# Kernel tuning notes

Hardware: AMD Instinct MI355X
Metric: run time of the kernel (lower is better)

## Reference

```python
import math
import jax, jax.numpy as jnp
import numpy as np

N_NODES = 50000
N_EDGES = 600000
D = 128          # in_dim == out_dim
T = 4            # num_types
R = 4            # num_relations
H = 8            # n_heads
DK = D // H
MAX_LEN = 240    # RelTemporalEncoding max_len
EPS = 1e-5


def _sinusoid_table(n_hid, max_len):
    pos = jnp.arange(max_len, dtype=jnp.float32)[:, None]
    div = jnp.exp(jnp.arange(0, n_hid, 2, dtype=jnp.float32) * (-math.log(10000.0) / n_hid))
    s = jnp.sin(pos * div) / math.sqrt(n_hid)
    c = jnp.cos(pos * div) / math.sqrt(n_hid)
    emb = jnp.zeros((max_len, n_hid), dtype=jnp.float32)
    emb = emb.at[:, 0::2].set(s).at[:, 1::2].set(c)
    return emb


def setup_inputs() -> dict:
    key = jax.random.key(0)
    ks = jax.random.split(key, 24)
    f32 = jnp.float32
    inp = {
        'node_inp': jax.random.normal(ks[0], (N_NODES, D), dtype=f32),
        'node_type': jax.random.randint(ks[1], (N_NODES,), 0, T),
        'edge_index': jax.random.randint(ks[2], (2, N_EDGES), 0, N_NODES),
        'edge_type': jax.random.randint(ks[3], (N_EDGES,), 0, R),
        'edge_time': jax.random.randint(ks[4], (N_EDGES,), 0, MAX_LEN),
        # per-type Linear weights stored as [T, in, out] (x @ W + b)
        'Wk': jax.random.normal(ks[5], (T, D, D), dtype=f32) * 0.05,
        'bk': jnp.zeros((T, D), dtype=f32),
        'Wq': jax.random.normal(ks[6], (T, D, D), dtype=f32) * 0.05,
        'bq': jnp.zeros((T, D), dtype=f32),
        'Wv': jax.random.normal(ks[7], (T, D, D), dtype=f32) * 0.05,
        'bv': jnp.zeros((T, D), dtype=f32),
        'Wa': jax.random.normal(ks[8], (T, D, D), dtype=f32) * 0.05,
        'ba': jnp.zeros((T, D), dtype=f32),
        'gamma': jnp.ones((T, D), dtype=f32),
        'beta': jnp.zeros((T, D), dtype=f32),
        'rel_pri': jnp.ones((R, H), dtype=f32),
        'rel_att': jax.random.normal(ks[9], (R, H, DK, DK), dtype=f32) * 0.1,
        'rel_msg': jax.random.normal(ks[10], (R, H, DK, DK), dtype=f32) * 0.1,
        'skip': jnp.ones((T,), dtype=f32),
        'rte_W': jax.random.normal(ks[11], (D, D), dtype=f32) * 0.05,
        'rte_b': jnp.zeros((D,), dtype=f32),
    }
    return inp


def _type_proj(x, W, b, types):
    # all-type projection [T, N, D] then gather per-node type (T is small)
    allp = jnp.einsum('ni,tio->tno', x, W) + b[:, None, :]
    return allp[types, jnp.arange(x.shape[0])]


def reference(node_inp, node_type, edge_index, edge_type, edge_time,
              Wk, bk, Wq, bq, Wv, bv, Wa, ba, gamma, beta,
              rel_pri, rel_att, rel_msg, skip, rte_W, rte_b):
    N = node_inp.shape[0]
    E = edge_index.shape[1]
    src, tgt = edge_index[0], edge_index[1]  # j (source) -> i (target)

    # --- RelTemporalEncoding: x + Linear(emb[t]); emb is a fixed sinusoid table
    rte_out = _sinusoid_table(D, MAX_LEN) @ rte_W + rte_b  # [240, D]

    # --- per-node type-specific K/Q/V (linearity: K_t(x + rte) = K_t(x) + rte @ Wk_t)
    k_node = _type_proj(node_inp, Wk, bk, node_type)  # [N, D]
    v_node = _type_proj(node_inp, Wv, bv, node_type)
    q_node = _type_proj(node_inp, Wq, bq, node_type)
    k_rte = jnp.einsum('mi,tio->tmo', rte_out, Wk)  # [T, 240, D] (no bias; already in k_node)
    v_rte = jnp.einsum('mi,tio->tmo', rte_out, Wv)

    stype = node_type[src]
    k_e = (k_node[src] + k_rte[stype, edge_time]).reshape(E, H, DK)
    v_e = (v_node[src] + v_rte[stype, edge_time]).reshape(E, H, DK)
    q_e = q_node[tgt].reshape(E, H, DK)

    # --- per-relation head-wise transforms (R is small, fixed loop)
    k2 = jnp.zeros_like(k_e)
    msg = jnp.zeros_like(v_e)
    for r in range(R):
        sel = (edge_type == r)[:, None, None]
        k2 = jnp.where(sel, jnp.einsum('ehk,hkd->ehd', k_e, rel_att[r]), k2)
        msg = jnp.where(sel, jnp.einsum('ehk,hkd->ehd', v_e, rel_msg[r]), msg)

    logits = (q_e * k2).sum(-1) * rel_pri[edge_type] / math.sqrt(DK)  # [E, H]

    # --- softmax over edges grouped by target node
    m = jax.ops.segment_max(logits, tgt, num_segments=N)
    ex = jnp.exp(logits - m[tgt])
    den = jax.ops.segment_sum(ex, tgt, num_segments=N)
    att = ex / den[tgt]  # [E, H]

    res = (msg * att[..., None]).reshape(E, D)
    aggr = jax.ops.segment_sum(res, tgt, num_segments=N)  # [N, D]

    # --- update: per-type FFN + gated skip + per-type LayerNorm
    a = jax.nn.gelu(aggr, approximate=False)
    trans = _type_proj(a, Wa, ba, node_type)  # dropout p used in eval mode -> identity
    alpha = jax.nn.sigmoid(skip)[node_type][:, None]
    h = trans * alpha + node_inp * (1.0 - alpha)
    mu = h.mean(-1, keepdims=True)
    var = ((h - mu) ** 2).mean(-1, keepdims=True)
    out = (h - mu) / jnp.sqrt(var + EPS) * gamma[node_type] + beta[node_type]
    return out
```

## Files before the change

### kernel.cpp

```cpp
#include <hip/hip_runtime.h>
#include <hip/hip_fp16.h>
#include <math.h>

#define NH 8
#define NT 4
#define NR 4
#define MAXLEN 240

typedef __attribute__((ext_vector_type(8))) short bf16x8;
typedef __attribute__((ext_vector_type(4))) float f32x4;
typedef __attribute__((ext_vector_type(2))) float f32x2;

#if defined(__has_builtin)
#if __has_builtin(__builtin_amdgcn_cvt_pk_f32_fp8) && __has_builtin(__builtin_amdgcn_cvt_pk_fp8_f32)
#define HAS_HW_FP8 1
#endif
#endif

__device__ __forceinline__ unsigned short f2bf(float x) {
    unsigned u = __float_as_uint(x);
    u += 0x7fffu + ((u >> 16) & 1u);
    return (unsigned short)(u >> 16);
}
__device__ __forceinline__ float bflo(unsigned u) { return __uint_as_float(u << 16); }
__device__ __forceinline__ float bfhi(unsigned u) { return __uint_as_float(u & 0xffff0000u); }
__device__ __forceinline__ unsigned pack2(float a, float b) {
    return (unsigned)f2bf(a) | ((unsigned)f2bf(b) << 16);
}

__device__ __forceinline__ void fp8x4_dec(unsigned w, float* f) {
#ifdef HAS_HW_FP8
    f32x2 lo = __builtin_amdgcn_cvt_pk_f32_fp8(w, false);
    f32x2 hi = __builtin_amdgcn_cvt_pk_f32_fp8(w, true);
    f[0] = lo[0]; f[1] = lo[1]; f[2] = hi[0]; f[3] = hi[1];
#else
    unsigned ev = w & 0x00ff00ffu;
    unsigned od = (w >> 8) & 0x00ff00ffu;
    unsigned he = (((ev << 8) & 0x80008000u) | ((ev << 7) & 0x3f803f80u)) + 0x04000400u;
    unsigned ho = (((od << 8) & 0x80008000u) | ((od << 7) & 0x3f803f80u)) + 0x04000400u;
    __half2 h2e = *reinterpret_cast<__half2*>(&he);
    __half2 h2o = *reinterpret_cast<__half2*>(&ho);
    float2 fe = __half22float2(h2e);
    float2 fo = __half22float2(h2o);
    f[0] = fe.x; f[1] = fo.x; f[2] = fe.y; f[3] = fo.y;
#endif
}
__device__ __forceinline__ unsigned fp8x2_enc(float a, float b) {
#ifdef HAS_HW_FP8
    return (unsigned)__builtin_amdgcn_cvt_pk_fp8_f32(a, b, 0, false) & 0xffffu;
#else
    auto enc1 = [](float x) -> unsigned {
        float cl = fminf(fmaxf(x, -448.f), 448.f);
        __half h = __float2half(cl * 0.00390625f);
        unsigned short hr = *reinterpret_cast<unsigned short*>(&h);
        unsigned short rnd = (unsigned short)((hr & 0x7fff) + 0x3f + ((hr >> 7) & 1));
        return (unsigned)(((rnd >> 7) & 0x7f) | ((hr >> 8) & 0x80));
    };
    return enc1(a) | (enc1(b) << 8);
#endif
}

__global__ void zero_kernel(int* deg, int* cursor, int* dcnt, int* dcur, int N) {
    int i = blockIdx.x * blockDim.x + threadIdx.x;
    int stride = gridDim.x * blockDim.x;
    if (i < 256) { dcnt[i] = 0; dcur[i] = 0; }
    for (int j = i; j < N; j += stride) { deg[j] = 0; cursor[j] = 0; }
}

__global__ void deg_kernel(const int* __restrict__ ei, int* __restrict__ deg, int E) {
    int i = blockIdx.x * blockDim.x + threadIdx.x;
    int stride = gridDim.x * blockDim.x;
    for (int e = i; e < E; e += stride) atomicAdd(&deg[ei[E + e]], 1);
}

__global__ __launch_bounds__(256) void histA(const int* __restrict__ ntype,
                                             const int* __restrict__ deg,
                                             int* __restrict__ dcnt, int N) {
    __shared__ int h[256];
    int tid = threadIdx.x;
    h[tid] = 0;
    __syncthreads();
    int i = blockIdx.x * 256 + tid;
    if (i < N) atomicAdd(&h[ntype[i] * 64 + 63 - min(deg[i], 63)], 1);
    __syncthreads();
    if (h[tid]) atomicAdd(&dcnt[tid], h[tid]);
}

__global__ __launch_bounds__(256) void histB(const int* __restrict__ dcnt,
                                             int* __restrict__ dbase) {
    __shared__ int tmp[256];
    int v = dcnt[threadIdx.x];
    tmp[threadIdx.x] = v;
    __syncthreads();
    #pragma unroll
    for (int off = 1; off < 256; off <<= 1) {
        int t = threadIdx.x >= off ? tmp[threadIdx.x - off] : 0;
        __syncthreads();
        tmp[threadIdx.x] += t;
        __syncthreads();
    }
    dbase[threadIdx.x] = tmp[threadIdx.x] - v;
}

__global__ __launch_bounds__(256) void histC(const int* __restrict__ ntype,
                                             const int* __restrict__ deg,
                                             const int* __restrict__ dbase, int* __restrict__ dcur,
                                             int* __restrict__ nlist, int* __restrict__ spos,
                                             int* __restrict__ stype_s, int* __restrict__ deg_s,
                                             int N) {
    __shared__ int h[256];
    __shared__ int bb[256];
    __shared__ int cur[256];
    int tid = threadIdx.x;
    h[tid] = 0; cur[tid] = 0;
    __syncthreads();
    int i = blockIdx.x * 256 + tid;
    int b = -1, t = 0, dg = 0;
    if (i < N) {
        t = ntype[i]; dg = deg[i];
        b = t * 64 + 63 - min(dg, 63);
        atomicAdd(&h[b], 1);
    }
    __syncthreads();
    if (h[tid]) bb[tid] = atomicAdd(&dcur[tid], h[tid]);
    __syncthreads();
    if (i < N) {
        int r = atomicAdd(&cur[b], 1);
        int p = dbase[b] + bb[b] + r;
        nlist[p] = i;
        spos[i] = p;
        stype_s[p] = t;
        deg_s[p] = dg;
    }
}

__global__ __launch_bounds__(256) void scanA(const int* __restrict__ deg, int* __restrict__ excl,
                                             int* __restrict__ bsum, int N) {
    __shared__ int tmp[256];
    int i = blockIdx.x * 256 + threadIdx.x;
    int v = i < N ? deg[i] : 0;
    tmp[threadIdx.x] = v;
    __syncthreads();
    #pragma unroll
    for (int off = 1; off < 256; off <<= 1) {
        int t = threadIdx.x >= off ? tmp[threadIdx.x - off] : 0;
        __syncthreads();
        tmp[threadIdx.x] += t;
        __syncthreads();
    }
    if (i < N) excl[i] = tmp[threadIdx.x] - v;
    if (threadIdx.x == 255) bsum[blockIdx.x] = tmp[255];
}

__global__ __launch_bounds__(256) void scanB(int* __restrict__ bsum, int nb) {
    __shared__ int tmp[256];
    int v = threadIdx.x < nb ? bsum[threadIdx.x] : 0;
    tmp[threadIdx.x] = v;
    __syncthreads();
    #pragma unroll
    for (int off = 1; off < 256; off <<= 1) {
        int t = threadIdx.x >= off ? tmp[threadIdx.x - off] : 0;
        __syncthreads();
        tmp[threadIdx.x] += t;
        __syncthreads();
    }
    if (threadIdx.x < nb) bsum[threadIdx.x] = tmp[threadIdx.x] - v;
}

__global__ void scanC(const int* __restrict__ excl, const int* __restrict__ bsum,
                      int* __restrict__ row_start, int N) {
    int i = blockIdx.x * blockDim.x + threadIdx.x;
    if (i < N) row_start[i] = excl[i] + bsum[i >> 8];
}

__global__ void scatter_kernel(const int* __restrict__ ei, const int* __restrict__ etype,
                               const int* __restrict__ etime, const int* __restrict__ spos,
                               const int* __restrict__ dbase,
                               const int* __restrict__ row_start, int* __restrict__ cursor,
                               unsigned* __restrict__ ebuf, int E) {
    int tb1 = dbase[64], tb2 = dbase[128], tb3 = dbase[192];
    int i = blockIdx.x * blockDim.x + threadIdx.x;
    int stride = gridDim.x * blockDim.x;
    for (int e = i; e < E; e += stride) {
        int sps = spos[ei[e]];
        int spt = spos[ei[E + e]];
        int st = (sps >= tb1) + (sps >= tb2) + (sps >= tb3);
        int pos = atomicAdd(&cursor[spt], 1);
        ebuf[row_start[spt] + pos] =
            (unsigned)sps | ((unsigned)etype[e] << 17) | ((unsigned)etime[e] << 19) | ((unsigned)st << 27);
    }
}

__global__ __launch_bounds__(128) void rte_tables(
    const float* __restrict__ rte_W, const float* __restrict__ rte_b,
    const float* __restrict__ Wk, const float* __restrict__ Wv,
    const float* __restrict__ rel_msg,
    unsigned char* __restrict__ rtec8) {
    int m = blockIdx.x, t = blockIdx.y, d = threadIdx.x;
    __shared__ float emb[128];
    __shared__ float sr[128];
    __shared__ float vr[128];
    int j2 = d & ~1;
    float div = expf((float)j2 * (-9.210340371976184f / 128.f));
    float ang = (float)m * div;
    emb[d] = ((d & 1) ? cosf(ang) : sinf(ang)) * 0.08838834764831845f;
    __syncthreads();
    float ro = rte_b[d];
    #pragma unroll 8
    for (int i = 0; i < 128; ++i) ro += emb[i] * rte_W[i * 128 + d];
    sr[d] = ro;
    __syncthreads();
    float ak = 0.f, av = 0.f;
    for (int i = 0; i < 128; ++i) {
        float rv = sr[i];
        ak += rv * Wk[(t * 128 + i) * 128 + d];
        av += rv * Wv[(t * 128 + i) * 128 + d];
    }
    unsigned char kb = (unsigned char)(fp8x2_enc(fminf(fmaxf(ak, -440.f), 440.f), 0.f) & 0xff);
    int koff = (d >> 3) * 16 + 8 + (d & 7);
    #pragma unroll
    for (int r = 0; r < NR; ++r)
        rtec8[(size_t)((t * 4 + r) * MAXLEN + m) * 256 + koff] = kb;
    vr[d] = av;
    __syncthreads();
    int h = d >> 4, dd = d & 15;
    int voff = (d >> 3) * 16 + (d & 7);
    for (int r = 0; r < NR; ++r) {
        float acc = 0.f;
        #pragma unroll
        for (int k = 0; k < 16; ++k)
            acc += vr[h * 16 + k] * rel_msg[((r * NH + h) * 16 + k) * 16 + dd];
        unsigned char vb = (unsigned char)(fp8x2_enc(fminf(fmaxf(acc, -440.f), 440.f), 0.f) & 0xff);
        rtec8[(size_t)((t * 4 + r) * MAXLEN + m) * 256 + voff] = vb;
    }
}

__global__ __launch_bounds__(256) void pack_w9(
    const float* __restrict__ Wk, const float* __restrict__ Wq,
    const float* __restrict__ Wv, const float* __restrict__ Wa,
    const float* __restrict__ bk, const float* __restrict__ bq,
    const float* __restrict__ bv, const float* __restrict__ ba,
    const float* __restrict__ rel_att, const float* __restrict__ rel_msg,
    const float* __restrict__ rel_pri,
    short* __restrict__ PW2, float* __restrict__ PB) {
    if (blockIdx.x >= 320) {
        int bidx = (blockIdx.x - 320) * 256 + threadIdx.x;
        int col = bidx & 127, t = (bidx >> 7) & 3, set = bidx >> 9;
        int h = col >> 4, kk = col & 15;
        float val;
        if (set == 0) val = bk[t * 128 + col];
        else if (set == 9) val = ba[t * 128 + col];
        else if (set <= 4) {
            int r = set - 1;
            float pri = rel_pri[r * NH + h] * 0.25f;
            float acc = 0.f;
            #pragma unroll
            for (int dp = 0; dp < 16; ++dp)
                acc += bq[t * 128 + h * 16 + dp] * rel_att[((r * NH + h) * 16 + kk) * 16 + dp];
            val = acc * pri;
        } else {
            int r = set - 5;
            float acc = 0.f;
            #pragma unroll
            for (int kp = 0; kp < 16; ++kp)
                acc += bv[t * 128 + h * 16 + kp] * rel_msg[((r * NH + h) * 16 + kp) * 16 + kk];
            val = acc;
        }
        PB[bidx] = val;
        return;
    }
    int idx = blockIdx.x * 256 + threadIdx.x;
    int lane = idx & 63;
    int ks = (idx >> 6) & 3;
    int ctg = (idx >> 8) & 7;
    int t = (idx >> 11) & 3;
    int set = idx >> 13;
    int col = ctg * 16 + (lane & 15);
    int k0 = ks * 32 + (lane >> 4) * 8;
    int h = col >> 4, kk = col & 15;
    unsigned short o[8];
    if (set == 0 || set == 9) {
        const float* W = (set == 0 ? Wk : Wa) + t * 16384;
        #pragma unroll
        for (int j = 0; j < 8; ++j) o[j] = f2bf(W[(k0 + j) * 128 + col]);
    } else if (set <= 4) {
        int r = set - 1;
        float pri = rel_pri[r * NH + h] * 0.25f;
        float Ar[16];
        #pragma unroll
        for (int dp = 0; dp < 16; ++dp)
            Ar[dp] = rel_att[((r * NH + h) * 16 + kk) * 16 + dp] * pri;
        #pragma unroll
        for (int j = 0; j < 8; ++j) {
            const float* wr = Wq + (size_t)(t * 128 + k0 + j) * 128 + h * 16;
            float acc = 0.f;
            #pragma unroll
            for (int dp = 0; dp < 16; ++dp) acc += wr[dp] * Ar[dp];
            o[j] = f2bf(acc);
        }
    } else {
        int r = set - 5;
        float Mc[16];
        #pragma unroll
        for (int kp = 0; kp < 16; ++kp)
            Mc[kp] = rel_msg[((r * NH + h) * 16 + kp) * 16 + kk];
        #pragma unroll
        for (int j = 0; j < 8; ++j) {
            const float* wr = Wv + (size_t)(t * 128 + k0 + j) * 128 + h * 16;
            float acc = 0.f;
            #pragma unroll
            for (int kp = 0; kp < 16; ++kp) acc += wr[kp] * Mc[kp];
            o[j] = f2bf(acc);
        }
    }
    uint4 pk;
    pk.x = (unsigned)o[0] | ((unsigned)o[1] << 16);
    pk.y = (unsigned)o[2] | ((unsigned)o[3] << 16);
    pk.z = (unsigned)o[4] | ((unsigned)o[5] << 16);
    pk.w = (unsigned)o[6] | ((unsigned)o[7] << 16);
    *reinterpret_cast<uint4*>(PW2 + (size_t)idx * 8) = pk;
}

#define S8 144
#define KST 144

__global__ __launch_bounds__(256, 4) void kqv2(
    const float* __restrict__ x, const int* __restrict__ nlist_,
    const int* __restrict__ stype_s, const short* __restrict__ PW2,
    const float* __restrict__ PB,
    unsigned char* __restrict__ knvm8, unsigned char* __restrict__ qa8, int N) {
    __shared__ short af_l[2][4][64][8];
    __shared__ unsigned char obuf[2][32 * S8];
    __shared__ unsigned char kn_keep[32 * KST];
    __shared__ int st_l[32];
    const int tid = threadIdx.x;
    const int sp0 = blockIdx.x * 32;
    if (tid < 32) {
        int sp = sp0 + tid;
        st_l[tid] = stype_s[sp < N ? sp : N - 1];
    }
    {
        int i = tid >> 3;
        int d0 = (tid & 7) * 16;
        int sp = sp0 + i;
        int nid = nlist_[sp < N ? sp : N - 1];
        const float* xr = x + (size_t)nid * 128 + d0;
        float4 f0 = *reinterpret_cast<const float4*>(xr);
        float4 f1 = *reinterpret_cast<const float4*>(xr + 4);
        float4 f2 = *reinterpret_cast<const float4*>(xr + 8);
        float4 f3 = *reinterpret_cast<const float4*>(xr + 12);
        int m = i >> 4, rr = i & 15;
        int ks = d0 >> 5;
        int sub = (d0 >> 3) & 3;
        uint4 p0, p1;
        p0.x = pack2(f0.x, f0.y); p0.y = pack2(f0.z, f0.w);
        p0.z = pack2(f1.x, f1.y); p0.w = pack2(f1.z, f1.w);
        p1.x = pack2(f2.x, f2.y); p1.y = pack2(f2.z, f2.w);
        p1.z = pack2(f3.x, f3.y); p1.w = pack2(f3.z, f3.w);
        *reinterpret_cast<uint4*>(&af_l[m][ks][sub * 16 + rr][0]) = p0;
        *reinterpret_cast<uint4*>(&af_l[m][ks][(sub + 1) * 16 + rr][0]) = p1;
    }
    __syncthreads();

    const int lane = tid & 63, w = tid >> 6;
    const int col_l = lane & 15, rowg = lane >> 4;
    const int t0 = st_l[0], t1 = st_l[31];

    bf16x8 afr[2][4];
    #pragma unroll
    for (int m = 0; m < 2; ++m)
        #pragma unroll
        for (int ks = 0; ks < 4; ++ks)
            afr[m][ks] = *reinterpret_cast<const bf16x8*>(&af_l[m][ks][lane][0]);

    const int wi = tid >> 3, wseg = tid & 7;
    const int wsp = sp0 + wi;

    for (int set = 0; set < 9; ++set) {
        unsigned char* buf = &obuf[set & 1][0];
        for (int t = t0; t <= t1; ++t) {
            #pragma unroll
            for (int c = 0; c < 2; ++c) {
                int ctg = w + c * 4;
                bf16x8 pf[4];
                #pragma unroll
                for (int ks = 0; ks < 4; ++ks)
                    pf[ks] = *reinterpret_cast<const bf16x8*>(
                        PW2 + ((size_t)((((set * 4 + t) * 8 + ctg) * 4 + ks) * 64 + lane)) * 8);
                float bval = PB[(set * 4 + t) * 128 + ctg * 16 + col_l];
                #pragma unroll
                for (int m = 0; m < 2; ++m) {
                    f32x4 acc = {0.f, 0.f, 0.f, 0.f};
                    #pragma unroll
                    for (int ks = 0; ks < 4; ++ks)
                        acc = __builtin_amdgcn_mfma_f32_16x16x32_bf16(afr[m][ks], pf[ks], acc, 0, 0, 0);
                    float c0 = fminf(fmaxf(acc[0] + bval, -440.f), 440.f);
                    float c1 = fminf(fmaxf(acc[1] + bval, -440.f), 440.f);
                    float c2 = fminf(fmaxf(acc[2] + bval, -440.f), 440.f);
                    float c3 = fminf(fmaxf(acc[3] + bval, -440.f), 440.f);
                    unsigned pA = fp8x2_enc(c0, c1);
                    unsigned pB = fp8x2_enc(c2, c3);
                    unsigned char by[4];
                    by[0] = (unsigned char)(pA & 0xff);
                    by[1] = (unsigned char)((pA >> 8) & 0xff);
                    by[2] = (unsigned char)(pB & 0xff);
                    by[3] = (unsigned char)((pB >> 8) & 0xff);
                    #pragma unroll
                    for (int j = 0; j < 4; ++j) {
                        int i = m * 16 + rowg * 4 + j;
                        if (st_l[i] == t)
                            buf[i * S8 + ctg * 16 + col_l] = by[j];
                    }
                }
            }
        }
        __syncthreads();
        if (set == 0) {
            *reinterpret_cast<uint4*>(&kn_keep[wi * KST + wseg * 16]) =
                *reinterpret_cast<const uint4*>(&buf[wi * S8 + wseg * 16]);
        } else if (set <= 4) {
            if (wsp < N) {
                int r = set - 1;
                *reinterpret_cast<uint4*>(qa8 + (size_t)(wsp * 4 + r) * 128 + wseg * 16) =
                    *reinterpret_cast<const uint4*>(&buf[wi * S8 + wseg * 16]);
            }
        } else {
            if (wsp < N) {
                int r = set - 5;
                unsigned char* dst = knvm8 + (size_t)(wsp * 4 + r) * 256;
                #pragma unroll
                for (int cc = 0; cc < 2; ++cc) {
                    int c = wseg * 2 + cc;
                    uint2 vmc = *reinterpret_cast<const uint2*>(&buf[wi * S8 + c * 8]);
                    uint2 knc = *reinterpret_cast<const uint2*>(&kn_keep[wi * KST + c * 8]);
                    uint4 outv;
                    outv.x = vmc.x; outv.y = vmc.y; outv.z = knc.x; outv.w = knc.y;
                    *reinterpret_cast<uint4*>(dst + c * 16) = outv;
                }
            }
        }
    }
}

__global__ __launch_bounds__(256) void fused_edge_attn(
    const unsigned* __restrict__ ebuf, const int* __restrict__ row_start,
    const int* __restrict__ deg_s,
    const unsigned char* __restrict__ knvm8, const unsigned char* __restrict__ rtec8,
    const unsigned char* __restrict__ qa8,
    unsigned short* __restrict__ aggr_bf, int N) {
    int sp = blockIdx.x * 16 + (threadIdx.x >> 4);
    int l16 = threadIdx.x & 15;
    if (sp >= N) return;
    uint4 q[4];
    #pragma unroll
    for (int r = 0; r < 4; ++r) {
        uint2 qv = *reinterpret_cast<const uint2*>(qa8 + (size_t)(sp * 4 + r) * 128 + l16 * 8);
        float f[8];
        fp8x4_dec(qv.x, f); fp8x4_dec(qv.y, f + 4);
        q[r].x = pack2(f[0], f[1]); q[r].y = pack2(f[2], f[3]);
        q[r].z = pack2(f[4], f[5]); q[r].w = pack2(f[6], f[7]);
    }
    int start = row_start[sp], cnt = deg_s[sp];
    float den = 0.f;
    float acc[8] = {0.f, 0.f, 0.f, 0.f, 0.f, 0.f, 0.f, 0.f};
    int i = 0;
    for (; i + 2 <= cnt; i += 2) {
        unsigned e0 = ebuf[start + i];
        unsigned e1 = ebuf[start + i + 1];
        int sps0 = e0 & 0x1ffff, r0 = (e0 >> 17) & 3, tm0 = (e0 >> 19) & 255, st0 = (e0 >> 27) & 3;
        int sps1 = e1 & 0x1ffff, r1 = (e1 >> 17) & 3, tm1 = (e1 >> 19) & 255, st1 = (e1 >> 27) & 3;
        uint4 g10 = *reinterpret_cast<const uint4*>(knvm8 + (size_t)(sps0 * 4 + r0) * 256 + l16 * 16);
        uint4 g20 = *reinterpret_cast<const uint4*>(rtec8 + (size_t)((st0 * 4 + r0) * MAXLEN + tm0) * 256 + l16 * 16);
        uint4 g11 = *reinterpret_cast<const uint4*>(knvm8 + (size_t)(sps1 * 4 + r1) * 256 + l16 * 16);
        uint4 g21 = *reinterpret_cast<const uint4*>(rtec8 + (size_t)((st1 * 4 + r1) * MAXLEN + tm1) * 256 + l16 * 16);
        float mf0[8], kf0[8], mr0[8], kr0[8];
        float mf1[8], kf1[8], mr1[8], kr1[8];
        fp8x4_dec(g10.x, mf0); fp8x4_dec(g10.y, mf0 + 4);
        fp8x4_dec(g10.z, kf0); fp8x4_dec(g10.w, kf0 + 4);
        fp8x4_dec(g20.x, mr0); fp8x4_dec(g20.y, mr0 + 4);
        fp8x4_dec(g20.z, kr0); fp8x4_dec(g20.w, kr0 + 4);
        fp8x4_dec(g11.x, mf1); fp8x4_dec(g11.y, mf1 + 4);
        fp8x4_dec(g11.z, kf1); fp8x4_dec(g11.w, kf1 + 4);
        fp8x4_dec(g21.x, mr1); fp8x4_dec(g21.y, mr1 + 4);
        fp8x4_dec(g21.z, kr1); fp8x4_dec(g21.w, kr1 + 4);
        uint4 q0 = q[r0], q1 = q[r1];
        float p0 = (kf0[0] + kr0[0]) * bflo(q0.x) + (kf0[1] + kr0[1]) * bfhi(q0.x)
                 + (kf0[2] + kr0[2]) * bflo(q0.y) + (kf0[3] + kr0[3]) * bfhi(q0.y)
                 + (kf0[4] + kr0[4]) * bflo(q0.z) + (kf0[5] + kr0[5]) * bfhi(q0.z)
                 + (kf0[6] + kr0[6]) * bflo(q0.w) + (kf0[7] + kr0[7]) * bfhi(q0.w);
        float p1 = (kf1[0] + kr1[0]) * bflo(q1.x) + (kf1[1] + kr1[1]) * bfhi(q1.x)
                 + (kf1[2] + kr1[2]) * bflo(q1.y) + (kf1[3] + kr1[3]) * bfhi(q1.y)
                 + (kf1[4] + kr1[4]) * bflo(q1.z) + (kf1[5] + kr1[5]) * bfhi(q1.z)
                 + (kf1[6] + kr1[6]) * bflo(q1.w) + (kf1[7] + kr1[7]) * bfhi(q1.w);
        p0 += __shfl_xor(p0, 1);
        p1 += __shfl_xor(p1, 1);
        float w0 = __expf(p0), w1 = __expf(p1);
        den += w0 + w1;
        #pragma unroll
        for (int j = 0; j < 8; ++j)
            acc[j] += w0 * (mf0[j] + mr0[j]) + w1 * (mf1[j] + mr1[j]);
    }
    if (i < cnt) {
        unsigned e0 = ebuf[start + i];
        int sps0 = e0 & 0x1ffff, r0 = (e0 >> 17) & 3, tm0 = (e0 >> 19) & 255, st0 = (e0 >> 27) & 3;
        uint4 g10 = *reinterpret_cast<const uint4*>(knvm8 + (size_t)(sps0 * 4 + r0) * 256 + l16 * 16);
        uint4 g20 = *reinterpret_cast<const uint4*>(rtec8 + (size_t)((st0 * 4 + r0) * MAXLEN + tm0) * 256 + l16 * 16);
        float mf0[8], kf0[8], mr0[8], kr0[8];
        fp8x4_dec(g10.x, mf0); fp8x4_dec(g10.y, mf0 + 4);
        fp8x4_dec(g10.z, kf0); fp8x4_dec(g10.w, kf0 + 4);
        fp8x4_dec(g20.x, mr0); fp8x4_dec(g20.y, mr0 + 4);
        fp8x4_dec(g20.z, kr0); fp8x4_dec(g20.w, kr0 + 4);
        uint4 q0 = q[r0];
        float p0 = (kf0[0] + kr0[0]) * bflo(q0.x) + (kf0[1] + kr0[1]) * bfhi(q0.x)
                 + (kf0[2] + kr0[2]) * bflo(q0.y) + (kf0[3] + kr0[3]) * bfhi(q0.y)
                 + (kf0[4] + kr0[4]) * bflo(q0.z) + (kf0[5] + kr0[5]) * bfhi(q0.z)
                 + (kf0[6] + kr0[6]) * bflo(q0.w) + (kf0[7] + kr0[7]) * bfhi(q0.w);
        p0 += __shfl_xor(p0, 1);
        float w0 = __expf(p0);
        den += w0;
        #pragma unroll
        for (int j = 0; j < 8; ++j)
            acc[j] += w0 * (mf0[j] + mr0[j]);
    }
    float inv = den > 0.f ? 1.f / den : 0.f;
    uint4 o;
    o.x = pack2(acc[0] * inv, acc[1] * inv);
    o.y = pack2(acc[2] * inv, acc[3] * inv);
    o.z = pack2(acc[4] * inv, acc[5] * inv);
    o.w = pack2(acc[6] * inv, acc[7] * inv);
    *reinterpret_cast<uint4*>(aggr_bf + (size_t)sp * 128 + l16 * 8) = o;
}

__global__ __launch_bounds__(256, 4) void update_sorted(
    const float* __restrict__ x, const int* __restrict__ nlist_,
    const int* __restrict__ stype_s, const short* __restrict__ PW2,
    const float* __restrict__ PB, const float* __restrict__ gamma,
    const float* __restrict__ beta, const float* __restrict__ skip,
    const unsigned short* __restrict__ aggr_bf, float* __restrict__ out, int N) {
    __shared__ short af_l[2][4][64][8];
    __shared__ float hs[32][128];
    __shared__ int st_l[32];
    __shared__ int nid_l[32];
    const int tid = threadIdx.x;
    const int sp0 = blockIdx.x * 32;
    if (tid < 32) {
        int sp = sp0 + tid;
        int spc = sp < N ? sp : N - 1;
        st_l[tid] = stype_s[spc];
        nid_l[tid] = nlist_[spc];
    }
    {
        int i = tid >> 3;
        int d0 = (tid & 7) * 16;
        int spc = sp0 + i < N ? sp0 + i : N - 1;
        const unsigned short* ar = aggr_bf + (size_t)spc * 128 + d0;
        uint4 v0 = *reinterpret_cast<const uint4*>(ar);
        uint4 v1 = *reinterpret_cast<const uint4*>(ar + 8);
        unsigned vv[8] = {v0.x, v0.y, v0.z, v0.w, v1.x, v1.y, v1.z, v1.w};
        float g[16];
        #pragma unroll
        for (int c = 0; c < 8; ++c) {
            float a0 = bflo(vv[c]), a1 = bfhi(vv[c]);
            g[c * 2 + 0] = 0.5f * a0 * (1.f + erff(a0 * 0.7071067811865476f));
            g[c * 2 + 1] = 0.5f * a1 * (1.f + erff(a1 * 0.7071067811865476f));
        }
        int m = i >> 4, rr = i & 15;
        int ks = d0 >> 5;
        int sub = (d0 >> 3) & 3;
        uint4 p0, p1;
        p0.x = pack2(g[0], g[1]);  p0.y = pack2(g[2], g[3]);
        p0.z = pack2(g[4], g[5]);  p0.w = pack2(g[6], g[7]);
        p1.x = pack2(g[8], g[9]);  p1.y = pack2(g[10], g[11]);
        p1.z = pack2(g[12], g[13]); p1.w = pack2(g[14], g[15]);
        *reinterpret_cast<uint4*>(&af_l[m][ks][sub * 16 + rr][0]) = p0;
        *reinterpret_cast<uint4*>(&af_l[m][ks][(sub + 1) * 16 + rr][0]) = p1;
    }
    __syncthreads();

    const int lane = tid & 63, w = tid >> 6;
    const int col_l = lane & 15, rowg = lane >> 4;
    const int t0 = st_l[0], t1 = st_l[31];

    bf16x8 afr[2][4];
    #pragma unroll
    for (int m = 0; m < 2; ++m)
        #pragma unroll
        for (int ks = 0; ks < 4; ++ks)
            afr[m][ks] = *reinterpret_cast<const bf16x8*>(&af_l[m][ks][lane][0]);

    for (int t = t0; t <= t1; ++t) {
        #pragma unroll
        for (int c = 0; c < 2; ++c) {
            int ctg = w + c * 4;
            bf16x8 pf[4];
            #pragma unroll
            for (int ks = 0; ks < 4; ++ks)
                pf[ks] = *reinterpret_cast<const bf16x8*>(
                    PW2 + ((size_t)((((9 * 4 + t) * 8 + ctg) * 4 + ks) * 64 + lane)) * 8);
            float bval = PB[(9 * 4 + t) * 128 + ctg * 16 + col_l];
            #pragma unroll
            for (int m = 0; m < 2; ++m) {
                f32x4 acc = {0.f, 0.f, 0.f, 0.f};
                #pragma unroll
                for (int ks = 0; ks < 4; ++ks)
                    acc = __builtin_amdgcn_mfma_f32_16x16x32_bf16(afr[m][ks], pf[ks], acc, 0, 0, 0);
                #pragma unroll
                for (int j = 0; j < 4; ++j) {
                    int i = m * 16 + rowg * 4 + j;
                    if (st_l[i] == t)
                        hs[i][ctg * 16 + col_l] = acc[j] + bval;
                }
            }
        }
    }
    __syncthreads();

    {
        int i = tid >> 3;
        int d0 = (tid & 7) * 16;
        int sp = sp0 + i;
        int nid = nid_l[i];
        int t = st_l[i];
        float alpha = 1.f / (1.f + expf(-skip[t]));
        const float* xr = x + (size_t)nid * 128 + d0;
        float hv[16];
        float s1 = 0.f, s2 = 0.f;
        #pragma unroll
        for (int c = 0; c < 4; ++c) {
            float4 xf = *reinterpret_cast<const float4*>(xr + c * 4);
            float4 tf;
            tf.x = hs[i][d0 + c * 4 + 0]; tf.y = hs[i][d0 + c * 4 + 1];
            tf.z = hs[i][d0 + c * 4 + 2]; tf.w = hs[i][d0 + c * 4 + 3];
            hv[c * 4 + 0] = tf.x * alpha + xf.x * (1.f - alpha);
            hv[c * 4 + 1] = tf.y * alpha + xf.y * (1.f - alpha);
            hv[c * 4 + 2] = tf.z * alpha + xf.z * (1.f - alpha);
            hv[c * 4 + 3] = tf.w * alpha + xf.w * (1.f - alpha);
            #pragma unroll
            for (int j = 0; j < 4; ++j) { s1 += hv[c * 4 + j]; s2 += hv[c * 4 + j] * hv[c * 4 + j]; }
        }
        #pragma unroll
        for (int off = 1; off < 8; off <<= 1) {
            s1 += __shfl_xor(s1, off);
            s2 += __shfl_xor(s2, off);
        }
        float mu = s1 * (1.f / 128.f);
        float var = s2 * (1.f / 128.f) - mu * mu;
        float inv = 1.f / sqrtf(var + 1e-5f);
        if (sp < N) {
            float* orow = out + (size_t)nid * 128 + d0;
            const float* gr = gamma + t * 128 + d0;
            const float* br = beta + t * 128 + d0;
            #pragma unroll
            for (int c = 0; c < 4; ++c) {
                float4 gf = *reinterpret_cast<const float4*>(gr + c * 4);
                float4 bf = *reinterpret_cast<const float4*>(br + c * 4);
                float4 of;
                of.x = (hv[c * 4 + 0] - mu) * inv * gf.x + bf.x;
                of.y = (hv[c * 4 + 1] - mu) * inv * gf.y + bf.y;
                of.z = (hv[c * 4 + 2] - mu) * inv * gf.z + bf.z;
                of.w = (hv[c * 4 + 3] - mu) * inv * gf.w + bf.w;
                *reinterpret_cast<float4*>(orow + c * 4) = of;
            }
        }
    }
}

extern "C" void kernel_launch(void* const* d_in, const int* in_sizes, int n_in,
                              void* d_out, int out_size, void* d_ws, size_t ws_size,
                              hipStream_t stream) {
    const float* node_inp = (const float*)d_in[0];
    const int*   node_type = (const int*)d_in[1];
    const int*   edge_index = (const int*)d_in[2];
    const int*   edge_type = (const int*)d_in[3];
    const int*   edge_time = (const int*)d_in[4];
    const float* Wk = (const float*)d_in[5];
    const float* bk = (const float*)d_in[6];
    const float* Wq = (const float*)d_in[7];
    const float* bq = (const float*)d_in[8];
    const float* Wv = (const float*)d_in[9];
    const float* bv = (const float*)d_in[10];
    const float* Wa = (const float*)d_in[11];
    const float* ba = (const float*)d_in[12];
    const float* gamma = (const float*)d_in[13];
    const float* beta = (const float*)d_in[14];
    const float* rel_pri = (const float*)d_in[15];
    const float* rel_att = (const float*)d_in[16];
    const float* rel_msg = (const float*)d_in[17];
    const float* skip = (const float*)d_in[18];
    const float* rte_W = (const float*)d_in[19];
    const float* rte_b = (const float*)d_in[20];

    int N = in_sizes[0] / 128;
    int E = in_sizes[3];

    char* base = (char*)d_ws;
    unsigned char* knvm8 = (unsigned char*)base;      base += (size_t)N * 4 * 256;
    unsigned char* qa8 = (unsigned char*)base;        base += (size_t)N * 4 * 128;
    unsigned short* aggr_bf = (unsigned short*)base;  base += (size_t)N * 128 * 2;
    unsigned char* rtec8 = (unsigned char*)base;      base += (size_t)NT * NR * MAXLEN * 256;
    short* PW2 = (short*)base;                base += (size_t)10 * NT * 128 * 128 * 2;
    float* PB = (float*)base;                 base += (size_t)10 * NT * 128 * 4;
    int* deg = (int*)base;                    base += (size_t)N * 4;
    int* deg_s = (int*)base;                  base += (size_t)N * 4;
    int* cursor = (int*)base;                 base += (size_t)N * 4;
    int* excl = (int*)base;                   base += (size_t)N * 4;
    int* row_start = (int*)base;              base += (size_t)N * 4;
    int* nlist = (int*)base;                  base += (size_t)N * 4;
    int* spos = (int*)base;                   base += (size_t)N * 4;
    int* stype_s = (int*)base;                base += (size_t)N * 4;
    int* bsum = (int*)base;                   base += 256 * 4;
    int* dcnt = (int*)base;                   base += 256 * 4;
    int* dcur = (int*)base;                   base += 256 * 4;
    int* dbase = (int*)base;                  base += 256 * 4;
    base = (char*)(((size_t)base + 15) & ~(size_t)15);
    unsigned* ebuf = (unsigned*)base;         base += (size_t)E * 4;

    int nb = (N + 255) / 256;
    int ng = (N + 255) / 256;

    zero_kernel<<<256, 256, 0, stream>>>(deg, cursor, dcnt, dcur, N);
    deg_kernel<<<1024, 256, 0, stream>>>(edge_index, deg, E);
    histA<<<ng, 256, 0, stream>>>(node_type, deg, dcnt, N);
    histB<<<1, 256, 0, stream>>>(dcnt, dbase);
    histC<<<ng, 256, 0, stream>>>(node_type, deg, dbase, dcur, nlist, spos, stype_s, deg_s, N);
    scanA<<<nb, 256, 0, stream>>>(deg_s, excl, bsum, N);
    scanB<<<1, 256, 0, stream>>>(bsum, nb);
    scanC<<<nb, 256, 0, stream>>>(excl, bsum, row_start, N);
    scatter_kernel<<<1024, 256, 0, stream>>>(edge_index, edge_type, edge_time, spos, dbase,
                                             row_start, cursor, ebuf, E);
    dim3 gt(MAXLEN, NT);
    rte_tables<<<gt, 128, 0, stream>>>(rte_W, rte_b, Wk, Wv, rel_msg, rtec8);
    pack_w9<<<340, 256, 0, stream>>>(Wk, Wq, Wv, Wa, bk, bq, bv, ba,
                                     rel_att, rel_msg, rel_pri, PW2, PB);
    kqv2<<<(N + 31) / 32, 256, 0, stream>>>(node_inp, nlist, stype_s, PW2, PB,
                                            knvm8, qa8, N);
    fused_edge_attn<<<(N + 15) / 16, 256, 0, stream>>>(ebuf, row_start, deg_s,
                                                       knvm8, rtec8, qa8, aggr_bf, N);
    update_sorted<<<(N + 31) / 32, 256, 0, stream>>>(node_inp, nlist, stype_s, PW2, PB,
                                                     gamma, beta, skip, aggr_bf, (float*)d_out, N);
}
```

Measured before the change: 217.1 us.

## Assign one wavefront per target node, splitting its edges over four slots

The edge attention kernel now maps a 64-lane wavefront to each target node instead of a 16-lane group. The four 16-lane slots stride over that node's edges, and their partial softmax denominators and accumulators are combined with cross-slot shuffles before slot 0 writes the result. The goal is more memory-level parallelism per node and less per-node serial latency, since degree averages about 12. The costs are four times as many blocks, redundant q loads and decoding in each slot, idle lanes on low-degree nodes, and extra shuffle reductions.

```diff
diff --git a/kernel.cpp b/kernel.cpp
--- a/kernel.cpp
+++ b/kernel.cpp
@@ -448,9 +448,11 @@
     const unsigned char* __restrict__ knvm8, const unsigned char* __restrict__ rtec8,
     const unsigned char* __restrict__ qa8,
     unsigned short* __restrict__ aggr_bf, int N) {
-    int sp = blockIdx.x * 16 + (threadIdx.x >> 4);
-    int l16 = threadIdx.x & 15;
+    int sp = blockIdx.x * 4 + (threadIdx.x >> 6);
     if (sp >= N) return;
+    int lane = threadIdx.x & 63;
+    int slot = lane >> 4;
+    int l16 = lane & 15;
     uint4 q[4];
     #pragma unroll
     for (int r = 0; r < 4; ++r) {
@@ -463,72 +465,44 @@
     int start = row_start[sp], cnt = deg_s[sp];
     float den = 0.f;
     float acc[8] = {0.f, 0.f, 0.f, 0.f, 0.f, 0.f, 0.f, 0.f};
-    int i = 0;
-    for (; i + 2 <= cnt; i += 2) {
-        unsigned e0 = ebuf[start + i];
-        unsigned e1 = ebuf[start + i + 1];
-        int sps0 = e0 & 0x1ffff, r0 = (e0 >> 17) & 3, tm0 = (e0 >> 19) & 255, st0 = (e0 >> 27) & 3;
-        int sps1 = e1 & 0x1ffff, r1 = (e1 >> 17) & 3, tm1 = (e1 >> 19) & 255, st1 = (e1 >> 27) & 3;
-        uint4 g10 = *reinterpret_cast<const uint4*>(knvm8 + (size_t)(sps0 * 4 + r0) * 256 + l16 * 16);
-        uint4 g20 = *reinterpret_cast<const uint4*>(rtec8 + (size_t)((st0 * 4 + r0) * MAXLEN + tm0) * 256 + l16 * 16);
-        uint4 g11 = *reinterpret_cast<const uint4*>(knvm8 + (size_t)(sps1 * 4 + r1) * 256 + l16 * 16);
-        uint4 g21 = *reinterpret_cast<const uint4*>(rtec8 + (size_t)((st1 * 4 + r1) * MAXLEN + tm1) * 256 + l16 * 16);
-        float mf0[8], kf0[8], mr0[8], kr0[8];
-        float mf1[8], kf1[8], mr1[8], kr1[8];
-        fp8x4_dec(g10.x, mf0); fp8x4_dec(g10.y, mf0 + 4);
-        fp8x4_dec(g10.z, kf0); fp8x4_dec(g10.w, kf0 + 4);
-        fp8x4_dec(g20.x, mr0); fp8x4_dec(g20.y, mr0 + 4);
-        fp8x4_dec(g20.z, kr0); fp8x4_dec(g20.w, kr0 + 4);
-        fp8x4_dec(g11.x, mf1); fp8x4_dec(g11.y, mf1 + 4);
-        fp8x4_dec(g11.z, kf1); fp8x4_dec(g11.w, kf1 + 4);
-        fp8x4_dec(g21.x, mr1); fp8x4_dec(g21.y, mr1 + 4);
-        fp8x4_dec(g21.z, kr1); fp8x4_dec(g21.w, kr1 + 4);
-        uint4 q0 = q[r0], q1 = q[r1];
-        float p0 = (kf0[0] + kr0[0]) * bflo(q0.x) + (kf0[1] + kr0[1]) * bfhi(q0.x)
-                 + (kf0[2] + kr0[2]) * bflo(q0.y) + (kf0[3] + kr0[3]) * bfhi(q0.y)
-                 + (kf0[4] + kr0[4]) * bflo(q0.z) + (kf0[5] + kr0[5]) * bfhi(q0.z)
-                 + (kf0[6] + kr0[6]) * bflo(q0.w) + (kf0[7] + kr0[7]) * bfhi(q0.w);
-        float p1 = (kf1[0] + kr1[0]) * bflo(q1.x) + (kf1[1] + kr1[1]) * bfhi(q1.x)
-                 + (kf1[2] + kr1[2]) * bflo(q1.y) + (kf1[3] + kr1[3]) * bfhi(q1.y)
-                 + (kf1[4] + kr1[4]) * bflo(q1.z) + (kf1[5] + kr1[5]) * bfhi(q1.z)
-                 + (kf1[6] + kr1[6]) * bflo(q1.w) + (kf1[7] + kr1[7]) * bfhi(q1.w);
-        p0 += __shfl_xor(p0, 1);
-        p1 += __shfl_xor(p1, 1);
-        float w0 = __expf(p0), w1 = __expf(p1);
-        den += w0 + w1;
-        #pragma unroll
-        for (int j = 0; j < 8; ++j)
-            acc[j] += w0 * (mf0[j] + mr0[j]) + w1 * (mf1[j] + mr1[j]);
-    }
-    if (i < cnt) {
+    for (int i = slot; i < cnt; i += 4) {
         unsigned e0 = ebuf[start + i];
         int sps0 = e0 & 0x1ffff, r0 = (e0 >> 17) & 3, tm0 = (e0 >> 19) & 255, st0 = (e0 >> 27) & 3;
-        uint4 g10 = *reinterpret_cast<const uint4*>(knvm8 + (size_t)(sps0 * 4 + r0) * 256 + l16 * 16);
-        uint4 g20 = *reinterpret_cast<const uint4*>(rtec8 + (size_t)((st0 * 4 + r0) * MAXLEN + tm0) * 256 + l16 * 16);
-        float mf0[8], kf0[8], mr0[8], kr0[8];
-        fp8x4_dec(g10.x, mf0); fp8x4_dec(g10.y, mf0 + 4);
-        fp8x4_dec(g10.z, kf0); fp8x4_dec(g10.w, kf0 + 4);
-        fp8x4_dec(g20.x, mr0); fp8x4_dec(g20.y, mr0 + 4);
-        fp8x4_dec(g20.z, kr0); fp8x4_dec(g20.w, kr0 + 4);
+        uint4 g1 = *reinterpret_cast<const uint4*>(knvm8 + (size_t)(sps0 * 4 + r0) * 256 + l16 * 16);
+        uint4 g2 = *reinterpret_cast<const uint4*>(rtec8 + (size_t)((st0 * 4 + r0) * MAXLEN + tm0) * 256 + l16 * 16);
+        float mf[8], kf[8], mr[8], kr[8];
+        fp8x4_dec(g1.x, mf); fp8x4_dec(g1.y, mf + 4);
+        fp8x4_dec(g1.z, kf); fp8x4_dec(g1.w, kf + 4);
+        fp8x4_dec(g2.x, mr); fp8x4_dec(g2.y, mr + 4);
+        fp8x4_dec(g2.z, kr); fp8x4_dec(g2.w, kr + 4);
         uint4 q0 = q[r0];
-        float p0 = (kf0[0] + kr0[0]) * bflo(q0.x) + (kf0[1] + kr0[1]) * bfhi(q0.x)
-                 + (kf0[2] + kr0[2]) * bflo(q0.y) + (kf0[3] + kr0[3]) * bfhi(q0.y)
-                 + (kf0[4] + kr0[4]) * bflo(q0.z) + (kf0[5] + kr0[5]) * bfhi(q0.z)
-                 + (kf0[6] + kr0[6]) * bflo(q0.w) + (kf0[7] + kr0[7]) * bfhi(q0.w);
-        p0 += __shfl_xor(p0, 1);
-        float w0 = __expf(p0);
+        float p = (kf[0] + kr[0]) * bflo(q0.x) + (kf[1] + kr[1]) * bfhi(q0.x)
+                + (kf[2] + kr[2]) * bflo(q0.y) + (kf[3] + kr[3]) * bfhi(q0.y)
+                + (kf[4] + kr[4]) * bflo(q0.z) + (kf[5] + kr[5]) * bfhi(q0.z)
+                + (kf[6] + kr[6]) * bflo(q0.w) + (kf[7] + kr[7]) * bfhi(q0.w);
+        p += __shfl_xor(p, 1);
+        float w0 = __expf(p);
         den += w0;
         #pragma unroll
         for (int j = 0; j < 8; ++j)
-            acc[j] += w0 * (mf0[j] + mr0[j]);
-    }
-    float inv = den > 0.f ? 1.f / den : 0.f;
-    uint4 o;
-    o.x = pack2(acc[0] * inv, acc[1] * inv);
-    o.y = pack2(acc[2] * inv, acc[3] * inv);
-    o.z = pack2(acc[4] * inv, acc[5] * inv);
-    o.w = pack2(acc[6] * inv, acc[7] * inv);
-    *reinterpret_cast<uint4*>(aggr_bf + (size_t)sp * 128 + l16 * 8) = o;
+            acc[j] += w0 * (mf[j] + mr[j]);
+    }
+    den += __shfl_xor(den, 16);
+    den += __shfl_xor(den, 32);
+    #pragma unroll
+    for (int j = 0; j < 8; ++j) {
+        acc[j] += __shfl_xor(acc[j], 16);
+        acc[j] += __shfl_xor(acc[j], 32);
+    }
+    if (slot == 0) {
+        float inv = den > 0.f ? 1.f / den : 0.f;
+        uint4 o;
+        o.x = pack2(acc[0] * inv, acc[1] * inv);
+        o.y = pack2(acc[2] * inv, acc[3] * inv);
+        o.z = pack2(acc[4] * inv, acc[5] * inv);
+        o.w = pack2(acc[6] * inv, acc[7] * inv);
+        *reinterpret_cast<uint4*>(aggr_bf + (size_t)sp * 128 + l16 * 8) = o;
+    }
 }
 
 __global__ __launch_bounds__(256, 4) void update_sorted(
@@ -734,8 +708,8 @@
                                      rel_att, rel_msg, rel_pri, PW2, PB);
     kqv2<<<(N + 31) / 32, 256, 0, stream>>>(node_inp, nlist, stype_s, PW2, PB,
                                             knvm8, qa8, N);
-    fused_edge_attn<<<(N + 15) / 16, 256, 0, stream>>>(ebuf, row_start, deg_s,
-                                                       knvm8, rtec8, qa8, aggr_bf, N);
+    fused_edge_attn<<<(N + 3) / 4, 256, 0, stream>>>(ebuf, row_start, deg_s,
+                                                     knvm8, rtec8, qa8, aggr_bf, N);
     update_sorted<<<(N + 31) / 32, 256, 0, stream>>>(node_inp, nlist, stype_s, PW2, PB,
                                                      gamma, beta, skip, aggr_bf, (float*)d_out, N);
 }
```

Result: slower. 239.4 us (+10.2%).
